# Kernel tuning notes

Hardware: AMD Instinct MI355X
Metric: run time of the kernel (lower is better)

## Reference

```python
import jax, jax.numpy as jnp
import numpy as np

N, C, T, VQ, VK = 8, 64, 256, 90, 50
S, L = 4, 4  # num_subset, lag_len
EPS = 1e-5


def conv1x1(x, W, b):
    # x: [n, c_in, t, v], W: [c_out, c_in], b: [c_out]
    return jnp.einsum('oc,nctv->notv', W, x) + b[None, :, None, None]


def batchnorm(x, gamma, beta):
    # training-mode BatchNorm2d with batch statistics (biased variance)
    m = jnp.mean(x, axis=(0, 2, 3), keepdims=True)
    v = jnp.mean((x - m) ** 2, axis=(0, 2, 3), keepdims=True)
    xn = (x - m) * jax.lax.rsqrt(v + EPS)
    return xn * gamma[None, :, None, None] + beta[None, :, None, None]


def setup_inputs() -> dict:
    key = jax.random.key(0)
    ks = jax.random.split(key, 20)
    f = lambda k, shp: jax.random.normal(k, shp, dtype=jnp.float32)
    w = 0.05
    return {
        'x_q': f(ks[0], (N, C, T, VQ)),
        'x_k': f(ks[1], (N, C, T, VK)),
        'x_v': f(ks[2], (N, C, T, VK)),
        'Wq': f(ks[3], (S * C, C)) * w, 'bq': f(ks[4], (S * C,)) * w,
        'Wk': f(ks[5], (S * C, C)) * w, 'bk': f(ks[6], (S * C,)) * w,
        'Wv': f(ks[7], (C, C)) * w, 'bv': f(ks[8], (C,)) * w,
        'Wout': f(ks[9], (C, S * C)) * w, 'bout': f(ks[10], (C,)) * w,
        'gamma_out': jnp.ones((C,), jnp.float32), 'beta_out': jnp.zeros((C,), jnp.float32),
        'Wdown': f(ks[11], (C, C)) * w, 'bdown': f(ks[12], (C,)) * w,
        'gamma_down': jnp.ones((C,), jnp.float32), 'beta_down': jnp.zeros((C,), jnp.float32),
    }


def reference(x_q, x_k, x_v, Wq, bq, Wk, bk, Wv, bv, Wout, bout,
              gamma_out, beta_out, Wdown, bdown, gamma_down, beta_down):
    Tq = T - L
    # query projection on truncated window -> [n, s, c, Tq, VQ]
    q = conv1x1(x_q[:, :, :Tq, :], Wq, bq).reshape(N, S, C, Tq, VQ)
    # 1x1 conv commutes with time slicing: project keys once over full T
    k_full = conv1x1(x_k, Wk, bk).reshape(N, S, C, T, VK)
    scale = (C * Tq) ** 0.5
    # multi-lag scores, each [n, s, VQ, VK]
    atts = [jnp.einsum('nsctu,nsctv->nsuv', q, k_full[:, :, :, l:Tq + l, :]) / scale
            for l in range(L + 1)]
    stack = jnp.stack(atts)  # [L+1, n, s, VQ, VK]
    p_att = (jnp.max(stack, axis=0) + jnp.mean(stack, axis=0)) * 0.5
    att = jax.nn.softmax(p_att, axis=-1)  # dropout = identity (eval)
    v = conv1x1(x_v, Wv, bv)  # [n, c, T, VK]
    y = jnp.einsum('nsvu,nctu->nsctv', att, v)  # [n, s, c, T, VQ]
    y = y.reshape(N, S * C, T, VQ)
    y = batchnorm(conv1x1(y, Wout, bout), gamma_out, beta_out)
    d = batchnorm(conv1x1(x_q, Wdown, bdown), gamma_down, beta_down)
    return jax.nn.leaky_relu(d + y, 0.1)
```

## Files before the change

### kernel.cpp

```cpp
#include <hip/hip_runtime.h>
#include <hip/hip_bf16.h>

typedef __hip_bfloat16 bf16;
typedef __attribute__((ext_vector_type(4))) short short4v;
typedef __attribute__((ext_vector_type(8))) short short8;
typedef __attribute__((ext_vector_type(16))) float f32x16;

__device__ __forceinline__ float b2f(bf16 x) { return __bfloat162float(x); }
__device__ __forceinline__ bf16  f2b(float x) { return __float2bfloat16(x); }
__device__ __forceinline__ short f2bs(float x) {
    bf16 h = __float2bfloat16(x);
    return *reinterpret_cast<short*>(&h);
}
__device__ __forceinline__ float s2f(short s) {
    bf16 h; *reinterpret_cast<short*>(&h) = s; return __bfloat162float(h);
}
__device__ __forceinline__ void gload_lds16(const void* g, void* l) {
    __builtin_amdgcn_global_load_lds(
        (const __attribute__((address_space(1))) void*)g,
        (__attribute__((address_space(3))) void*)l, 16, 0, 0);
}

constexpr int N_ = 8, C_ = 64, T_ = 256, VQ_ = 90, VK_ = 50, S_ = 4, L_ = 4;
constexpr int Tq_ = T_ - L_;
constexpr int NL  = L_ + 1;
constexpr int COLS = T_ * VQ_;
constexpr float EPSf = 1e-5f;
constexpr int NSL = 16;

__global__ __launch_bounds__(64)
void k0_precompute(const float* __restrict__ Wq, const float* __restrict__ bq,
                   const float* __restrict__ Wk, const float* __restrict__ bk,
                   short* __restrict__ MtA, float* __restrict__ bMp,
                   float* __restrict__ wb, float* __restrict__ cb) {
    int s  = blockIdx.x >> 6;
    int ci = blockIdx.x & 63;
    int cj = threadIdx.x;
    float m = 0.f;
    for (int c = 0; c < C_; ++c)
        m += Wq[(s * C_ + c) * C_ + ci] * Wk[(s * C_ + c) * C_ + cj];
    MtA[((cj >> 3) * 256 + s * C_ + ci) * 8 + (cj & 7)] = f2bs(m);
    if (cj == 0) {
        float v = 0.f;
        for (int c = 0; c < C_; ++c)
            v += Wq[(s * C_ + c) * C_ + ci] * bk[s * C_ + c];
        bMp[s * C_ + ci] = v;
    }
    if (ci == 0) {
        float v = 0.f;
        for (int c = 0; c < C_; ++c)
            v += bq[s * C_ + c] * Wk[(s * C_ + c) * C_ + cj];
        wb[s * C_ + cj] = v;
        if (cj == 0) {
            float v2 = 0.f;
            for (int c = 0; c < C_; ++c)
                v2 += bq[s * C_ + c] * bk[s * C_ + c];
            cb[s] = v2;
        }
    }
}

__global__ __launch_bounds__(256)
void k0b_wos(const float* __restrict__ Wout, const float* __restrict__ bout,
             const float* __restrict__ Wv, const float* __restrict__ bv,
             short* __restrict__ WosA, float* __restrict__ bos) {
    int cj = blockIdx.x;
    __shared__ float wvcol[C_];
    if (threadIdx.x < C_) wvcol[threadIdx.x] = Wv[threadIdx.x * C_ + cj];
    __syncthreads();
    int p = threadIdx.x;
    int s = p >> 6, o = p & 63;
    float acc = 0.f;
    for (int c = 0; c < C_; ++c)
        acc += Wout[o * (S_ * C_) + s * C_ + c] * wvcol[c];
    WosA[((cj >> 3) * 256 + p) * 8 + (cj & 7)] = f2bs(acc);
    if (cj == 0 && p < C_) {
        float a = bout[p];
        for (int k = 0; k < S_ * C_; ++k)
            a += Wout[p * (S_ * C_) + k] * bv[k & 63];
        bos[p] = a;
    }
}

__global__ __launch_bounds__(256)
void k0c_xqt(const float* __restrict__ xq, short* __restrict__ xqT) {
    int tt = blockIdx.x;
    int g  = blockIdx.y;
    int n  = blockIdx.z;
    int t0 = tt * 4;
    __shared__ float lds[8 * 360];
    int tid = threadIdx.x;
    const float* src = xq + ((size_t)(n * 64 + g * 8) * 256 + t0) * 90;
#pragma unroll
    for (int i = tid; i < 720; i += 256) {
        int c = i / 90, r = i % 90;
        float4 v = *(const float4*)(src + (size_t)c * 23040 + r * 4);
        *(float4*)(&lds[c * 360 + r * 4]) = v;
    }
    __syncthreads();
    for (int e = tid; e < 4 * 96; e += 256) {
        int t = e / 96, u = e % 96;
        short8 pk;
#pragma unroll
        for (int j = 0; j < 8; ++j)
            pk[j] = (u < 90) ? f2bs(lds[j * 360 + t * 90 + u]) : (short)0;
        *(short8*)(xqT + (((size_t)(n * 8 + g) * 256 + t0 + t) * 96 + u) * 8) = pk;
    }
}

__global__ __launch_bounds__(256)
void k1_mfma(const float* __restrict__ x_k, const short* __restrict__ MtA,
             const float* __restrict__ bMp, short* __restrict__ kqT) {
    int tb = blockIdx.x, n = blockIdx.y;
    int t0 = tb * 2;
    __shared__ __align__(16) short Ab[8 * 256 * 8];
    __shared__ __align__(16) short Bb[8 * 128 * 8];
    __shared__ float bmp_s[256];
    __shared__ float xs[3200];
    int tid = threadIdx.x;
    int wave = tid >> 6, lane = tid & 63, q = lane >> 5, c32 = lane & 31;
    if (tid < 256) bmp_s[tid] = bMp[tid];
    {
        const short8* Asrc = (const short8*)MtA;
#pragma unroll
        for (int it = 0; it < 8; ++it) {
            int call = wave * 8 + it;
            gload_lds16(Asrc + call * 64 + lane, (char*)Ab + call * 1024);
        }
    }
#pragma unroll
    for (int p = 0; p < 2; ++p) {
        for (int i4 = tid; i4 < 800; i4 += 256) {
            int cc = i4 / 25, o = i4 % 25;
            *(float4*)(&xs[cc * 100 + o * 4]) =
                *(const float4*)(x_k + ((size_t)(n * 64 + p * 32 + cc) * 256 + t0) * 50 + o * 4);
        }
        __syncthreads();
        for (int m = tid; m < 512; m += 256) {
            int kgl = m >> 7, c = m & 127, t = c >> 6, v = c & 63;
            short8 pk;
            if (v < VK_) {
#pragma unroll
                for (int j = 0; j < 8; ++j) pk[j] = f2bs(xs[(kgl * 8 + j) * 100 + t * 50 + v]);
            } else {
#pragma unroll
                for (int j = 0; j < 8; ++j) pk[j] = 0;
            }
            *(short8*)(Bb + ((p * 4 + kgl) * 128 + c) * 8) = pk;
        }
        __syncthreads();
    }
    asm volatile("s_waitcnt vmcnt(0)" ::: "memory");
    __builtin_amdgcn_s_barrier();
    f32x16 acc[2][4];
#pragma unroll
    for (int mt = 0; mt < 2; ++mt) {
#pragma unroll
        for (int r = 0; r < 16; ++r) {
            float b = bmp_s[wave * 64 + mt * 32 + (r & 3) + 8 * (r >> 2) + 4 * q];
#pragma unroll
            for (int nt = 0; nt < 4; ++nt) acc[mt][nt][r] = b;
        }
    }
#pragma unroll
    for (int ks = 0; ks < 4; ++ks) {
        int kg = 2 * ks + q;
        short8 a0 = *(const short8*)(Ab + (kg * 256 + wave * 64 + c32) * 8);
        short8 a1 = *(const short8*)(Ab + (kg * 256 + wave * 64 + 32 + c32) * 8);
#pragma unroll
        for (int nt = 0; nt < 4; ++nt) {
            short8 b = *(const short8*)(Bb + (kg * 128 + nt * 32 + c32) * 8);
            acc[0][nt] = __builtin_amdgcn_mfma_f32_32x32x16_bf16(a0, b, acc[0][nt], 0, 0, 0);
            acc[1][nt] = __builtin_amdgcn_mfma_f32_32x32x16_bf16(a1, b, acc[1][nt], 0, 0, 0);
        }
    }
    int ns = n * 4 + wave;
#pragma unroll
    for (int mt = 0; mt < 2; ++mt)
#pragma unroll
        for (int nt = 0; nt < 4; ++nt) {
            int t = nt >> 1, v = (nt & 1) * 32 + c32;
            if (v < VK_) {
                f32x16 A = acc[mt][nt];
#pragma unroll
                for (int rq = 0; rq < 4; ++rq) {
                    short4v pk;
#pragma unroll
                    for (int rr = 0; rr < 4; ++rr) pk[rr] = f2bs(A[rq * 4 + rr]);
                    *(short4v*)(kqT + ((((size_t)(ns * 8 + mt * 4 + rq)) * 256 + t0 + t) * VK_ + v) * 8 + 4 * q) = pk;
                }
            }
        }
}

__global__ __launch_bounds__(128)
void k3b_kbsum(const float* __restrict__ x_k, const float* __restrict__ wb,
               const float* __restrict__ cb, float* __restrict__ kbsum) {
    int cjg = blockIdx.x;
    int n = blockIdx.y;
    __shared__ float S[2][NL][VK_];
    for (int pr = threadIdx.x; pr < 2 * VK_; pr += 128) {
        int cjl = pr / VK_, v = pr % VK_;
        const float* base = x_k + ((size_t)(n * 64 + cjg * 2 + cjl) * 256) * VK_ + v;
        float a = 0.f;
        for (int t = 0; t < Tq_; ++t) a += base[t * VK_];
        S[cjl][0][v] = a;
        float run = a;
        for (int l = 1; l < NL; ++l) {
            run += base[(251 + l) * VK_] - base[(l - 1) * VK_];
            S[cjl][l][v] = run;
        }
    }
    __syncthreads();
    for (int e = threadIdx.x; e < S_ * NL * VK_; e += 128) {
        int s = e / (NL * VK_), r = e % (NL * VK_), l = r / VK_, v = r % VK_;
        float a = wb[s * 64 + cjg * 2] * S[0][l][v] + wb[s * 64 + cjg * 2 + 1] * S[1][l][v];
        if (cjg == 0) a += (float)Tq_ * cb[s];
        atomicAdd(&kbsum[((size_t)(n * 4 + s) * NL + l) * VK_ + v], a);
    }
}

__global__ __launch_bounds__(256)
void k3_mfma(const short* __restrict__ xqT, const short* __restrict__ kqT,
             float* __restrict__ partial) {
    int lin = blockIdx.x + 16 * blockIdx.y;
    int grp = lin & 7;
    int idx = lin >> 3;
    int slice = grp + 8 * (idx >> 3);
    int sub = idx & 7;
    int n = slice >> 3, g = slice & 7;
    int s = sub >> 1, half = sub & 1;
    int ns = n * 4 + s;
    int gx = g * 2 + half;
    __shared__ __align__(16) short sbuf[2][15872];
    int tid = threadIdx.x;
    int wave = tid >> 6, lane = tid & 63;
    int q = lane >> 5, nl = lane & 31;
    int n1 = wave * 64 + nl, n2 = n1 + 32;
    int nc1 = min(n1, 249), nc2 = min(n2, 249);
    int l1 = nc1 / VK_, v1 = nc1 % VK_;
    int l2 = nc2 / VK_, v2 = nc2 % VK_;
    int bo1 = ((q + l1) * VK_ + v1) * 8;
    int bo2 = ((q + l2) * VK_ + v2) * 8;
    int ao = (q * 96 + nl) * 8;
    f32x16 acc[6];
#pragma unroll
    for (int i = 0; i < 6; ++i)
#pragma unroll
        for (int r = 0; r < 16; ++r) acc[i][r] = 0.f;
    const short* asrc = xqT + (size_t)(n * 8 + g) * 256 * 768;
    const short* bsrc = kqT + (size_t)(ns * 8 + g) * 256 * 400;
    int c0 = half * 10, nch = half ? 11 : 10;
    int ncall = (wave == 3) ? 7 : 8;

    auto stage = [&](int buf, int ch) {
        int t0 = ch * 12;
        const short8* aS = (const short8*)(asrc + t0 * 768);
        const short8* bS = (const short8*)(bsrc + t0 * 400);
        char* db = (char*)(&sbuf[buf][0]);
        for (int it = 0; it < ncall; ++it) {
            int call = wave * 8 + it;
            int i = call * 64 + lane;
            const void* gsrc = (i < 1152) ? (const void*)(aS + i)
                                          : (const void*)(bS + min(i - 1152, 799));
            gload_lds16(gsrc, db + call * 1024);
        }
    };

    stage(0, c0);
    for (int ci = 0; ci < nch; ++ci) {
        int cur = ci & 1;
        if (ci + 1 < nch) {
            stage(cur ^ 1, c0 + ci + 1);
            if (wave == 3) asm volatile("s_waitcnt vmcnt(7)" ::: "memory");
            else           asm volatile("s_waitcnt vmcnt(8)" ::: "memory");
        } else {
            asm volatile("s_waitcnt vmcnt(0)" ::: "memory");
        }
        __builtin_amdgcn_s_barrier();
        const short* xa  = &sbuf[cur][0];
        const short* kbs = &sbuf[cur][9216];
        __builtin_amdgcn_s_setprio(1);
#pragma unroll
        for (int ts = 0; ts < 6; ++ts) {
            short8 a0 = *(const short8*)(xa + ao + ts * 1536);
            short8 a1 = *(const short8*)(xa + ao + 256 + ts * 1536);
            short8 a2 = *(const short8*)(xa + ao + 512 + ts * 1536);
            short8 b0 = *(const short8*)(kbs + bo1 + ts * 800);
            short8 b1 = *(const short8*)(kbs + bo2 + ts * 800);
            acc[0] = __builtin_amdgcn_mfma_f32_32x32x16_bf16(a0, b0, acc[0], 0, 0, 0);
            acc[1] = __builtin_amdgcn_mfma_f32_32x32x16_bf16(a1, b0, acc[1], 0, 0, 0);
            acc[2] = __builtin_amdgcn_mfma_f32_32x32x16_bf16(a2, b0, acc[2], 0, 0, 0);
            acc[3] = __builtin_amdgcn_mfma_f32_32x32x16_bf16(a0, b1, acc[3], 0, 0, 0);
            acc[4] = __builtin_amdgcn_mfma_f32_32x32x16_bf16(a1, b1, acc[4], 0, 0, 0);
            acc[5] = __builtin_amdgcn_mfma_f32_32x32x16_bf16(a2, b1, acc[5], 0, 0, 0);
        }
        __builtin_amdgcn_s_setprio(0);
        __builtin_amdgcn_s_barrier();
    }
#pragma unroll
    for (int inb = 0; inb < 2; ++inb) {
        int ng = wave * 64 + inb * 32 + nl;
        if (ng < 250) {
            int l = ng / VK_, v = ng % VK_;
            float* pb = partial + (((size_t)(ns * 5 + l) * NSL + gx) * 90) * VK_ + v;
#pragma unroll
            for (int iu = 0; iu < 3; ++iu) {
#pragma unroll
                for (int r = 0; r < 16; ++r) {
                    int u2 = iu * 32 + (r & 3) + 8 * (r >> 2) + 4 * q;
                    if (u2 < 90) pb[(size_t)u2 * VK_] = acc[inb * 3 + iu][r];
                }
            }
        }
    }
}

__global__ __launch_bounds__(256)
void k4_softmax(const float* __restrict__ partial, const float* __restrict__ kbsum,
                bf16* __restrict__ att) {
    int ug = blockIdx.x;
    int ns = blockIdx.y;
    int u0 = ug * 15;
    __shared__ float sred[NL * 15 * VK_];
    for (int idx = threadIdx.x; idx < NL * 15 * VK_; idx += 256) {
        int l = idx / (15 * VK_), r = idx % (15 * VK_);
        int u2 = r / VK_, v = r % VK_;
        const float* p = partial + ((size_t)(ns * NL + l) * NSL) * 90 * VK_
                         + (u0 + u2) * VK_ + v;
        float a = 0.f;
#pragma unroll
        for (int sl = 0; sl < NSL; ++sl) a += p[(size_t)sl * 90 * VK_];
        sred[idx] = a;
    }
    __syncthreads();
    if (threadIdx.x < 15) {
        int u2 = threadIdx.x;
        const float inv_scale = rsqrtf((float)(C_ * Tq_));
        float pv[VK_];
        float pmax = -1e30f;
#pragma unroll
        for (int v = 0; v < VK_; ++v) {
            float mx = -1e30f, mn = 0.f;
#pragma unroll
            for (int l = 0; l < NL; ++l) {
                float sl = (sred[(l * 15 + u2) * VK_ + v] + kbsum[((size_t)ns * NL + l) * VK_ + v]) * inv_scale;
                mx = fmaxf(mx, sl); mn += sl;
            }
            pv[v] = 0.5f * (mx + mn * (1.f / NL));
            pmax = fmaxf(pmax, pv[v]);
        }
        float sum = 0.f;
#pragma unroll
        for (int v = 0; v < VK_; ++v) { pv[v] = __expf(pv[v] - pmax); sum += pv[v]; }
        float inv = 1.f / sum;
#pragma unroll
        for (int v = 0; v < VK_; ++v)
            att[((size_t)ns * VQ_ + u0 + u2) * VK_ + v] = f2b(pv[v] * inv);
    }
}

__global__ __launch_bounds__(256)
void k5_mfma(const float* __restrict__ x_v, const short* __restrict__ WosA,
             short* __restrict__ wv_pack) {
    int tb = blockIdx.x, n = blockIdx.y;
    int t0 = tb * 2;
    __shared__ __align__(16) short Ab[8 * 256 * 8];
    __shared__ __align__(16) short Bb[8 * 128 * 8];
    __shared__ float xs[3200];
    int tid = threadIdx.x;
    int wave = tid >> 6, lane = tid & 63, q = lane >> 5, c32 = lane & 31;
    {
        const short8* Asrc = (const short8*)WosA;
#pragma unroll
        for (int it = 0; it < 8; ++it) {
            int call = wave * 8 + it;
            gload_lds16(Asrc + call * 64 + lane, (char*)Ab + call * 1024);
        }
    }
#pragma unroll
    for (int p = 0; p < 2; ++p) {
        for (int i4 = tid; i4 < 800; i4 += 256) {
            int cc = i4 / 25, o = i4 % 25;
            *(float4*)(&xs[cc * 100 + o * 4]) =
                *(const float4*)(x_v + ((size_t)(n * 64 + p * 32 + cc) * 256 + t0) * 50 + o * 4);
        }
        __syncthreads();
        for (int m = tid; m < 512; m += 256) {
            int kgl = m >> 7, c = m & 127, t = c >> 6, v = c & 63;
            short8 pk;
            if (v < VK_) {
#pragma unroll
                for (int j = 0; j < 8; ++j) pk[j] = f2bs(xs[(kgl * 8 + j) * 100 + t * 50 + v]);
            } else {
#pragma unroll
                for (int j = 0; j < 8; ++j) pk[j] = 0;
            }
            *(short8*)(Bb + ((p * 4 + kgl) * 128 + c) * 8) = pk;
        }
        __syncthreads();
    }
    asm volatile("s_waitcnt vmcnt(0)" ::: "memory");
    __builtin_amdgcn_s_barrier();
    f32x16 acc[4][2];
#pragma unroll
    for (int m = 0; m < 4; ++m)
#pragma unroll
        for (int nn2 = 0; nn2 < 2; ++nn2)
#pragma unroll
            for (int r = 0; r < 16; ++r) acc[m][nn2][r] = 0.f;
#pragma unroll
    for (int ks = 0; ks < 4; ++ks) {
        int kg = 2 * ks + q;
        short8 bw0 = *(const short8*)(Ab + (kg * 256 + wave * 64 + c32) * 8);
        short8 bw1 = *(const short8*)(Ab + (kg * 256 + wave * 64 + 32 + c32) * 8);
#pragma unroll
        for (int m = 0; m < 4; ++m) {
            short8 ax = *(const short8*)(Bb + (kg * 128 + m * 32 + c32) * 8);
            acc[m][0] = __builtin_amdgcn_mfma_f32_32x32x16_bf16(ax, bw0, acc[m][0], 0, 0, 0);
            acc[m][1] = __builtin_amdgcn_mfma_f32_32x32x16_bf16(ax, bw1, acc[m][1], 0, 0, 0);
        }
    }
#pragma unroll
    for (int m = 0; m < 4; ++m)
#pragma unroll
        for (int nn2 = 0; nn2 < 2; ++nn2) {
            int o = nn2 * 32 + c32;
            int t = t0 + (m >> 1);
            f32x16 A = acc[m][nn2];
            size_t base = (((size_t)(n * 256 + t) * 32) + wave * 8 + (m & 1) * 4) * 512 + o * 8 + 4 * q;
#pragma unroll
            for (int rq = 0; rq < 4; ++rq) {
                short4v pk;
#pragma unroll
                for (int rr = 0; rr < 4; ++rr) pk[rr] = f2bs(A[rq * 4 + rr]);
                *(short4v*)(wv_pack + base + (size_t)rq * 512) = pk;
            }
        }
}

__global__ __launch_bounds__(256)
void k6_mfma(const bf16* __restrict__ att, const short* __restrict__ wv_pack,
             const float* __restrict__ bos, bf16* __restrict__ out_pre) {
    int tc = blockIdx.x, n = blockIdx.y;
    __shared__ __align__(16) short att_p[32 * 96 * 8];
    __shared__ float bos_s[64];
    int tid = threadIdx.x;
    if (tid < 64) bos_s[tid] = bos[tid];
    for (int m = tid; m < 96 * 256; m += 256) {
        int u2 = m >> 8, k = m & 255;
        int s = k >> 6, vs = k & 63;
        short val = 0;
        if (u2 < 90 && vs < VK_) {
            bf16 h = att[((size_t)(n * 4 + s) * 90 + u2) * VK_ + vs];
            val = *reinterpret_cast<short*>(&h);
        }
        att_p[((k >> 3) * 96 + u2) * 8 + (k & 7)] = val;
    }
    __syncthreads();
    int wave = tid >> 6, lane = tid & 63;
    int q = lane >> 5, c = lane & 31;
    int t = tc * 4 + wave;
    f32x16 acc[6];
#pragma unroll
    for (int ot = 0; ot < 2; ++ot)
#pragma unroll
        for (int r = 0; r < 16; ++r) {
            float b = bos_s[ot * 32 + (r & 3) + 8 * (r >> 2) + 4 * q];
            acc[ot * 3 + 0][r] = b; acc[ot * 3 + 1][r] = b; acc[ot * 3 + 2][r] = b;
        }
    const short* wbase = wv_pack + (size_t)(n * 256 + t) * (32 * 512);
#pragma unroll
    for (int st = 0; st < 16; ++st) {
        int gq = 2 * st + q;
        short8 a0 = *(const short8*)(wbase + (gq * 64 + c) * 8);
        short8 a1 = *(const short8*)(wbase + (gq * 64 + 32 + c) * 8);
        short8 b0 = *(const short8*)(att_p + (gq * 96 + c) * 8);
        short8 b1 = *(const short8*)(att_p + (gq * 96 + 32 + c) * 8);
        short8 b2 = *(const short8*)(att_p + (gq * 96 + 64 + c) * 8);
        acc[0] = __builtin_amdgcn_mfma_f32_32x32x16_bf16(a0, b0, acc[0], 0, 0, 0);
        acc[1] = __builtin_amdgcn_mfma_f32_32x32x16_bf16(a0, b1, acc[1], 0, 0, 0);
        acc[2] = __builtin_amdgcn_mfma_f32_32x32x16_bf16(a0, b2, acc[2], 0, 0, 0);
        acc[3] = __builtin_amdgcn_mfma_f32_32x32x16_bf16(a1, b0, acc[3], 0, 0, 0);
        acc[4] = __builtin_amdgcn_mfma_f32_32x32x16_bf16(a1, b1, acc[4], 0, 0, 0);
        acc[5] = __builtin_amdgcn_mfma_f32_32x32x16_bf16(a1, b2, acc[5], 0, 0, 0);
    }
#pragma unroll
    for (int ot = 0; ot < 2; ++ot)
#pragma unroll
        for (int ut = 0; ut < 3; ++ut) {
            int u2 = ut * 32 + c;
            if (u2 < 90) {
                f32x16 A = acc[ot * 3 + ut];
#pragma unroll
                for (int r = 0; r < 16; ++r) {
                    int o = ot * 32 + (r & 3) + 8 * (r >> 2) + 4 * q;
                    out_pre[((size_t)(n * 64 + o) * 256 + t) * 90 + u2] = f2b(A[r]);
                }
            }
        }
}

__global__ __launch_bounds__(256)
void k7_mfma(const float* __restrict__ X, const float* __restrict__ W,
             const float* __restrict__ bias, bf16* __restrict__ out) {
    int cb = blockIdx.x, n = blockIdx.y;
    int col0 = cb * 256;
    __shared__ __align__(16) short A[8 * 64 * 8];
    __shared__ __align__(16) short B[8 * 256 * 8];
    __shared__ float bias_s[64];
    __shared__ float xs[2048];
    int tid = threadIdx.x;
    if (tid < 64) bias_s[tid] = bias[tid];
    for (int idx = tid; idx < 4096; idx += 256) {
        int o = idx >> 6, k = idx & 63;
        A[((k >> 3) * 64 + o) * 8 + (k & 7)] = f2bs(W[o * 64 + k]);
    }
#pragma unroll
    for (int p = 0; p < 8; ++p) {
        for (int i4 = tid; i4 < 512; i4 += 256) {
            int cl = i4 >> 6, o = i4 & 63;
            *(float4*)(&xs[cl * 256 + o * 4]) =
                *(const float4*)(X + (size_t)(n * 64 + p * 8 + cl) * COLS + col0 + o * 4);
        }
        __syncthreads();
        {
            short8 pk;
#pragma unroll
            for (int j = 0; j < 8; ++j) pk[j] = f2bs(xs[j * 256 + tid]);
            *(short8*)(B + (p * 256 + tid) * 8) = pk;
        }
        __syncthreads();
    }
    int wave = tid >> 6, lane = tid & 63, q = lane >> 5, c32 = lane & 31;
    f32x16 acc[2][2];
#pragma unroll
    for (int mt = 0; mt < 2; ++mt)
#pragma unroll
        for (int r = 0; r < 16; ++r) {
            float b = bias_s[mt * 32 + (r & 3) + 8 * (r >> 2) + 4 * q];
            acc[mt][0][r] = b; acc[mt][1][r] = b;
        }
#pragma unroll
    for (int ks = 0; ks < 4; ++ks) {
        int kg = 2 * ks + q;
        short8 a0 = *(const short8*)(A + (kg * 64 + c32) * 8);
        short8 a1 = *(const short8*)(A + (kg * 64 + 32 + c32) * 8);
#pragma unroll
        for (int i = 0; i < 2; ++i) {
            short8 b = *(const short8*)(B + (kg * 256 + (wave * 2 + i) * 32 + c32) * 8);
            acc[0][i] = __builtin_amdgcn_mfma_f32_32x32x16_bf16(a0, b, acc[0][i], 0, 0, 0);
            acc[1][i] = __builtin_amdgcn_mfma_f32_32x32x16_bf16(a1, b, acc[1][i], 0, 0, 0);
        }
    }
#pragma unroll
    for (int mt = 0; mt < 2; ++mt)
#pragma unroll
        for (int i = 0; i < 2; ++i) {
            int col = col0 + (wave * 2 + i) * 32 + c32;
#pragma unroll
            for (int r = 0; r < 16; ++r) {
                int o = mt * 32 + (r & 3) + 8 * (r >> 2) + 4 * q;
                out[(size_t)(n * 64 + o) * COLS + col] = f2b(acc[mt][i][r]);
            }
        }
}

__global__ __launch_bounds__(256)
void k8_stats(const bf16* __restrict__ out_pre, const bf16* __restrict__ d_pre,
              float* __restrict__ stats) {
    int path = blockIdx.x >> 9;
    int b = blockIdx.x & 511;
    int o = b >> 3, n = b & 7;
    const bf16* p = (path ? d_pre : out_pre) + ((size_t)n * C_ + o) * COLS;
    float s = 0.f, sq = 0.f;
    for (int i8 = threadIdx.x; i8 < COLS / 8; i8 += 256) {
        short8 v8 = *(const short8*)(p + i8 * 8);
#pragma unroll
        for (int j = 0; j < 8; ++j) {
            float x = s2f(v8[j]);
            s += x; sq += x * x;
        }
    }
#pragma unroll
    for (int off = 32; off > 0; off >>= 1) {
        s  += __shfl_down(s, off, 64);
        sq += __shfl_down(sq, off, 64);
    }
    __shared__ float red[8];
    int wid = threadIdx.x >> 6, lane = threadIdx.x & 63;
    if (lane == 0) { red[wid * 2] = s; red[wid * 2 + 1] = sq; }
    __syncthreads();
    if (threadIdx.x == 0) {
        float S = 0.f, Q = 0.f;
        for (int w2 = 0; w2 < 4; ++w2) { S += red[w2 * 2]; Q += red[w2 * 2 + 1]; }
        atomicAdd(&stats[path * 128 + o * 2], S);
        atomicAdd(&stats[path * 128 + o * 2 + 1], Q);
    }
}

__global__ __launch_bounds__(256)
void k9_final(const bf16* __restrict__ out_pre, const bf16* __restrict__ d_pre,
              const float* __restrict__ stats,
              const float* __restrict__ gamma_out, const float* __restrict__ beta_out,
              const float* __restrict__ gamma_down, const float* __restrict__ beta_down,
              float* __restrict__ out) {
    const float invM = 1.f / ((float)N_ * COLS);
    size_t total8 = (size_t)N_ * C_ * COLS / 8;
    size_t stride = (size_t)gridDim.x * blockDim.x;
    for (size_t i8 = (size_t)blockIdx.x * blockDim.x + threadIdx.x; i8 < total8; i8 += stride) {
        size_t idx = i8 * 8;
        int o = (int)((idx / COLS) % C_);
        float my = stats[o * 2] * invM;
        float vy = stats[o * 2 + 1] * invM - my * my;
        float md = stats[128 + o * 2] * invM;
        float vd = stats[128 + o * 2 + 1] * invM - md * md;
        float ay = rsqrtf(vy + EPSf) * gamma_out[o];
        float by = beta_out[o] - my * ay;
        float ad = rsqrtf(vd + EPSf) * gamma_down[o];
        float bd = beta_down[o] - md * ad;
        short8 y8 = *(const short8*)(out_pre + idx);
        short8 d8 = *(const short8*)(d_pre + idx);
        float rr[8];
#pragma unroll
        for (int j = 0; j < 8; ++j) {
            float r = (s2f(y8[j]) * ay + by) + (s2f(d8[j]) * ad + bd);
            rr[j] = r > 0.f ? r : 0.1f * r;
        }
        *(float4*)(out + idx)     = make_float4(rr[0], rr[1], rr[2], rr[3]);
        *(float4*)(out + idx + 4) = make_float4(rr[4], rr[5], rr[6], rr[7]);
    }
}

extern "C" void kernel_launch(void* const* d_in, const int* in_sizes, int n_in,
                              void* d_out, int out_size, void* d_ws, size_t ws_size,
                              hipStream_t stream) {
    (void)in_sizes; (void)n_in; (void)out_size; (void)ws_size;
    const float* x_q  = (const float*)d_in[0];
    const float* x_k  = (const float*)d_in[1];
    const float* x_v  = (const float*)d_in[2];
    const float* Wq   = (const float*)d_in[3];
    const float* bq   = (const float*)d_in[4];
    const float* Wk   = (const float*)d_in[5];
    const float* bk   = (const float*)d_in[6];
    const float* Wv   = (const float*)d_in[7];
    const float* bv   = (const float*)d_in[8];
    const float* Wout = (const float*)d_in[9];
    const float* bout = (const float*)d_in[10];
    const float* gamma_out  = (const float*)d_in[11];
    const float* beta_out   = (const float*)d_in[12];
    const float* Wdown = (const float*)d_in[13];
    const float* bdown = (const float*)d_in[14];
    const float* gamma_down = (const float*)d_in[15];
    const float* beta_down  = (const float*)d_in[16];

    char* w = (char*)d_ws;
    size_t off = 0;
    auto nxt = [&](size_t bytes) {
        char* p = w + off;
        off += (bytes + 255) & ~(size_t)255;
        return p;
    };
    short* MtA   = (short*)nxt((size_t)8 * 256 * 8 * 2);
    float* bMp   = (float*)nxt(256 * 4);
    float* wbp   = (float*)nxt((size_t)S_ * C_ * 4);
    float* cbp   = (float*)nxt((size_t)S_ * 4);
    short* WosA  = (short*)nxt((size_t)8 * 256 * 8 * 2);
    float* bos   = (float*)nxt((size_t)C_ * 4);
    float* kbsum = (float*)nxt((size_t)N_ * S_ * NL * VK_ * 4);
    bf16*  att   = (bf16*)nxt((size_t)N_ * S_ * VQ_ * VK_ * 2);
    float* stats = (float*)nxt(256 * 4);
    char* regionA = nxt((size_t)N_ * 8 * T_ * 96 * 8 * 2);
    short* xqT    = (short*)regionA;
    bf16*  out_pre = (bf16*)regionA;
    char* regionB = nxt((size_t)N_ * S_ * 8 * T_ * VK_ * 8 * 2);
    short* kqT   = (short*)regionB;
    bf16*  d_pre = (bf16*)regionB;
    char* regionC = nxt((size_t)N_ * T_ * 32 * 512 * 2);
    float* partial = (float*)regionC;
    short* wv_pack = (short*)regionC;

    hipMemsetAsync(stats, 0, 256 * 4, stream);
    hipMemsetAsync(kbsum, 0, (size_t)N_ * S_ * NL * VK_ * 4, stream);

    k0_precompute<<<S_ * C_, 64, 0, stream>>>(Wq, bq, Wk, bk, MtA, bMp, wbp, cbp);
    k0b_wos<<<C_, 256, 0, stream>>>(Wout, bout, Wv, bv, WosA, bos);
    k0c_xqt<<<dim3(64, 8, N_), 256, 0, stream>>>(x_q, xqT);
    k1_mfma<<<dim3(128, N_), 256, 0, stream>>>(x_k, MtA, bMp, kqT);
    k3b_kbsum<<<dim3(32, N_), 128, 0, stream>>>(x_k, wbp, cbp, kbsum);
    k3_mfma<<<dim3(NSL, N_ * S_), 256, 0, stream>>>(xqT, kqT, partial);
    k4_softmax<<<dim3(6, N_ * S_), 256, 0, stream>>>(partial, kbsum, att);
    k5_mfma<<<dim3(128, N_), 256, 0, stream>>>(x_v, WosA, wv_pack);
    k6_mfma<<<dim3(T_ / 4, N_), 256, 0, stream>>>(att, wv_pack, bos, out_pre);
    k7_mfma<<<dim3(COLS / 256, N_), 256, 0, stream>>>(x_q, Wdown, bdown, d_pre);
    k8_stats<<<1024, 256, 0, stream>>>(out_pre, d_pre, stats);
    k9_final<<<2880, 256, 0, stream>>>(out_pre, d_pre, stats, gamma_out, beta_out,
                                       gamma_down, beta_down, (float*)d_out);
}
```

Before: 368.4 us.

## Pre-pack attention in MFMA layout and stage k6 output through LDS

The softmax kernel now writes attention probabilities directly in the packed k-major layout that k6 consumes. This lets k6 load its attention tile with direct global-to-LDS 16-byte copies instead of a scalar gather-and-repack loop. k6 also transposes its accumulators through LDS so each output row is written with 16-byte vector stores rather than scattered 2-byte stores. The cost is an extra memset of the packed buffer, whose zero padding is needed, plus extra barriers and LDS traffic in k6.

```diff
diff --git a/kernel.cpp b/kernel.cpp
--- a/kernel.cpp
+++ b/kernel.cpp
@@ -318,7 +318,7 @@
 
 __global__ __launch_bounds__(256)
 void k4_softmax(const float* __restrict__ partial, const float* __restrict__ kbsum,
-                bf16* __restrict__ att) {
+                short* __restrict__ att_pk) {
     int ug = blockIdx.x;
     int ns = blockIdx.y;
     int u0 = ug * 15;
@@ -354,9 +354,11 @@
 #pragma unroll
         for (int v = 0; v < VK_; ++v) { pv[v] = __expf(pv[v] - pmax); sum += pv[v]; }
         float inv = 1.f / sum;
+        int n = ns >> 2, s = ns & 3;
+        short* base = att_pk + ((size_t)(n * 32 + s * 8)) * 96 * 8;
 #pragma unroll
         for (int v = 0; v < VK_; ++v)
-            att[((size_t)ns * VQ_ + u0 + u2) * VK_ + v] = f2b(pv[v] * inv);
+            base[(size_t)((v >> 3) * 96 + (u0 + u2)) * 8 + (v & 7)] = f2bs(pv[v] * inv);
     }
 }
 
@@ -440,26 +442,25 @@
 }
 
 __global__ __launch_bounds__(256)
-void k6_mfma(const bf16* __restrict__ att, const short* __restrict__ wv_pack,
+void k6_mfma(const short* __restrict__ att_pk, const short* __restrict__ wv_pack,
              const float* __restrict__ bos, bf16* __restrict__ out_pre) {
     int tc = blockIdx.x, n = blockIdx.y;
     __shared__ __align__(16) short att_p[32 * 96 * 8];
     __shared__ float bos_s[64];
     int tid = threadIdx.x;
-    if (tid < 64) bos_s[tid] = bos[tid];
-    for (int m = tid; m < 96 * 256; m += 256) {
-        int u2 = m >> 8, k = m & 255;
-        int s = k >> 6, vs = k & 63;
-        short val = 0;
-        if (u2 < 90 && vs < VK_) {
-            bf16 h = att[((size_t)(n * 4 + s) * 90 + u2) * VK_ + vs];
-            val = *reinterpret_cast<short*>(&h);
-        }
-        att_p[((k >> 3) * 96 + u2) * 8 + (k & 7)] = val;
-    }
-    __syncthreads();
     int wave = tid >> 6, lane = tid & 63;
     int q = lane >> 5, c = lane & 31;
+    if (tid < 64) bos_s[tid] = bos[tid];
+    {
+        const short8* src = (const short8*)(att_pk + (size_t)n * 24576);
+#pragma unroll
+        for (int it = 0; it < 12; ++it) {
+            int call = wave * 12 + it;
+            gload_lds16(src + call * 64 + lane, (char*)att_p + call * 1024);
+        }
+    }
+    asm volatile("s_waitcnt vmcnt(0)" ::: "memory");
+    __syncthreads();
     int t = tc * 4 + wave;
     f32x16 acc[6];
 #pragma unroll
@@ -485,20 +486,31 @@
         acc[4] = __builtin_amdgcn_mfma_f32_32x32x16_bf16(a1, b1, acc[4], 0, 0, 0);
         acc[5] = __builtin_amdgcn_mfma_f32_32x32x16_bf16(a1, b2, acc[5], 0, 0, 0);
     }
+    __syncthreads();
+    short* tw = att_p + wave * 6144;
 #pragma unroll
     for (int ot = 0; ot < 2; ++ot)
 #pragma unroll
         for (int ut = 0; ut < 3; ++ut) {
             int u2 = ut * 32 + c;
-            if (u2 < 90) {
-                f32x16 A = acc[ot * 3 + ut];
-#pragma unroll
-                for (int r = 0; r < 16; ++r) {
-                    int o = ot * 32 + (r & 3) + 8 * (r >> 2) + 4 * q;
-                    out_pre[((size_t)(n * 64 + o) * 256 + t) * 90 + u2] = f2b(A[r]);
-                }
+            f32x16 A = acc[ot * 3 + ut];
+#pragma unroll
+            for (int r = 0; r < 16; ++r) {
+                int o = ot * 32 + (r & 3) + 8 * (r >> 2) + 4 * q;
+                tw[o * 96 + u2] = f2bs(A[r]);
             }
         }
+    __syncthreads();
+    bf16* obase = out_pre + ((size_t)(n * 64) * 256 + t) * 90;
+#pragma unroll
+    for (int i = 0; i < 12; ++i) {
+        int unit = i * 64 + lane;
+        int o = unit / 12, u8 = unit % 12;
+        bf16* dst = obase + (size_t)o * 256 * 90 + u8 * 8;
+        const short* srcl = tw + o * 96 + u8 * 8;
+        if (u8 < 11) *(short8*)dst = *(const short8*)srcl;
+        else         *(int*)dst = *(const int*)srcl;
+    }
 }
 
 __global__ __launch_bounds__(256)
@@ -668,7 +680,7 @@
     short* WosA  = (short*)nxt((size_t)8 * 256 * 8 * 2);
     float* bos   = (float*)nxt((size_t)C_ * 4);
     float* kbsum = (float*)nxt((size_t)N_ * S_ * NL * VK_ * 4);
-    bf16*  att   = (bf16*)nxt((size_t)N_ * S_ * VQ_ * VK_ * 2);
+    short* att_pk = (short*)nxt((size_t)N_ * 32 * 96 * 8 * 2);
     float* stats = (float*)nxt(256 * 4);
     char* regionA = nxt((size_t)N_ * 8 * T_ * 96 * 8 * 2);
     short* xqT    = (short*)regionA;
@@ -682,6 +694,7 @@
 
     hipMemsetAsync(stats, 0, 256 * 4, stream);
     hipMemsetAsync(kbsum, 0, (size_t)N_ * S_ * NL * VK_ * 4, stream);
+    hipMemsetAsync(att_pk, 0, (size_t)N_ * 32 * 96 * 8 * 2, stream);
 
     k0_precompute<<<S_ * C_, 64, 0, stream>>>(Wq, bq, Wk, bk, MtA, bMp, wbp, cbp);
     k0b_wos<<<C_, 256, 0, stream>>>(Wout, bout, Wv, bv, WosA, bos);
@@ -689,9 +702,9 @@
     k1_mfma<<<dim3(128, N_), 256, 0, stream>>>(x_k, MtA, bMp, kqT);
     k3b_kbsum<<<dim3(32, N_), 128, 0, stream>>>(x_k, wbp, cbp, kbsum);
     k3_mfma<<<dim3(NSL, N_ * S_), 256, 0, stream>>>(xqT, kqT, partial);
-    k4_softmax<<<dim3(6, N_ * S_), 256, 0, stream>>>(partial, kbsum, att);
+    k4_softmax<<<dim3(6, N_ * S_), 256, 0, stream>>>(partial, kbsum, att_pk);
     k5_mfma<<<dim3(128, N_), 256, 0, stream>>>(x_v, WosA, wv_pack);
-    k6_mfma<<<dim3(T_ / 4, N_), 256, 0, stream>>>(att, wv_pack, bos, out_pre);
+    k6_mfma<<<dim3(T_ / 4, N_), 256, 0, stream>>>(att_pk, wv_pack, bos, out_pre);
     k7_mfma<<<dim3(COLS / 256, N_), 256, 0, stream>>>(x_q, Wdown, bdown, d_pre);
     k8_stats<<<1024, 256, 0, stream>>>(out_pre, d_pre, stats);
     k9_final<<<2880, 256, 0, stream>>>(out_pre, d_pre, stats, gamma_out, beta_out,
```

Result: faster. 347.9 us (-5.6%).
